# Performance work log

Hardware: AMD Instinct MI355X
Metric: run time of the kernel (lower is better)

Reference implementation:

```python
import jax, jax.numpy as jnp
import numpy as np

B, T, H, CH = 8192, 10, 512, 512  # batch, time_step, hidden_size, code_hidden_size (must be equal)


def setup_inputs() -> dict:
    key = jax.random.key(0)
    ks = jax.random.split(key, 18)
    s = 0.05
    inp = {
        "h": jax.random.normal(ks[0], (B, T, CH), dtype=jnp.float32),
        "y_seq": jax.random.normal(ks[1], (B, T), dtype=jnp.float32),
        "attn1_w": jax.random.normal(ks[2], (CH, 2 * H), dtype=jnp.float32) * s,
        "attn1_b": jax.random.normal(ks[3], (CH,), dtype=jnp.float32) * s,
        "attn2_w": jax.random.normal(ks[4], (CH, CH), dtype=jnp.float32) * s,
        "attn2_b": jax.random.normal(ks[5], (CH,), dtype=jnp.float32) * s,
        "attn3_w": jax.random.normal(ks[6], (1, CH), dtype=jnp.float32) * s,
        "attn3_b": jax.random.normal(ks[7], (1,), dtype=jnp.float32) * s,
        "W_ih": jax.random.normal(ks[8], (4 * H, 1), dtype=jnp.float32) * s,
        "W_hh": jax.random.normal(ks[9], (4 * H, H), dtype=jnp.float32) * s,
        "b_ih": jax.random.normal(ks[10], (4 * H,), dtype=jnp.float32) * s,
        "b_hh": jax.random.normal(ks[11], (4 * H,), dtype=jnp.float32) * s,
        "fc1_w": jax.random.normal(ks[12], (H, CH + H), dtype=jnp.float32) * s,
        "fc1_b": jax.random.normal(ks[13], (H,), dtype=jnp.float32) * s,
        "fc2_w": jax.random.normal(ks[14], (1, H), dtype=jnp.float32) * s,
        "fc2_b": jax.random.normal(ks[15], (1,), dtype=jnp.float32) * s,
    }
    return inp


def reference(h, y_seq, attn1_w, attn1_b, attn2_w, attn2_b, attn3_w, attn3_b,
              W_ih, W_hh, b_ih, b_hh, fc1_w, fc1_b, fc2_w, fc2_b):
    # h: [B, T, CH] -> scan over time; y_seq: [B, T]
    h_t = jnp.transpose(h, (1, 0, 2))      # [T, B, CH]
    y_t = jnp.transpose(y_seq, (1, 0))     # [T, B]
    b = h.shape[0]
    hid = W_hh.shape[1]
    d0 = jnp.zeros((b, hid), dtype=h.dtype)
    s0 = jnp.zeros((b, hid), dtype=h.dtype)

    def step(carry, xs):
        d, s = carry
        ht, yt = xs  # ht: [B, CH], yt: [B]
        # attention scores (note: original softmax is over a singleton dim -> weights == 1)
        x = jnp.concatenate([d, ht], axis=1)                       # [B, 2H]
        a = jnp.tanh((x @ attn1_w.T + attn1_b) @ attn2_w.T + attn2_b)
        w = a @ attn3_w.T + attn3_b                                # [B, 1]
        w = jax.nn.softmax(w, axis=1)                              # softmax over size-1 dim == 1
        h1 = w * ht                                                # [B, H] (CH == H)
        # single LSTM step with h0 = h1, c0 = s, input = yt (scalar feature)
        gates = yt[:, None] @ W_ih.T + b_ih + h1 @ W_hh.T + b_hh   # [B, 4H]
        i, f, g, o = jnp.split(gates, 4, axis=1)
        c = jax.nn.sigmoid(f) * s + jax.nn.sigmoid(i) * jnp.tanh(g)
        d_new = jax.nn.sigmoid(o) * jnp.tanh(c)
        return (d_new, c), None

    (d, s), _ = jax.lax.scan(step, (d0, s0), (h_t, y_t))
    z = jnp.concatenate([d, h_t[-1]], axis=1)                      # [B, CH+H]
    y_res = (z @ fc1_w.T + fc1_b) @ fc2_w.T + fc2_b                # [B, 1]
    return y_res
```

## Files before the change

kernel.cpp:

```cpp
#include <hip/hip_runtime.h>
#include <stdint.h>

typedef __attribute__((ext_vector_type(8))) short short8;
typedef __attribute__((ext_vector_type(4))) float f32x4;
typedef unsigned short ushort_t;

#define T_STEPS 10
#define BT  128
#define JPB 128
#define WPACK_BYTES (2048*1024)
#define VBUF_OFF  WPACK_BYTES
#define HBF_OFF   (WPACK_BYTES + 8192)
#define H_ELEMS   (8192ull*T_STEPS*512)
#define HBF_BYTES (H_ELEMS*2)

typedef const __attribute__((address_space(1))) void gas_void;
typedef __attribute__((address_space(3))) void las_void;

__device__ __forceinline__ void gld_lds16(const void* g, void* l){
  __builtin_amdgcn_global_load_lds((gas_void*)g, (las_void*)l, 16, 0, 0);
}

__device__ __forceinline__ unsigned int pk2(float x, float y){
  unsigned int bx = __float_as_uint(x), by = __float_as_uint(y);
  bx = (bx + 0x7FFFu + ((bx>>16)&1u)) >> 16;
  by = (by + 0x7FFFu + ((by>>16)&1u)) >> 16;
  return bx | (by<<16);
}
__device__ __forceinline__ float sigf(float x){ return 1.f/(1.f + __expf(-x)); }
__device__ __forceinline__ float tanh_(float x){
  x = fminf(fmaxf(x, -15.f), 15.f);
  float e = __expf(2.f*x);
  return (e - 1.f)/(e + 1.f);
}

__global__ __launch_bounds__(256) void k_pack(const float* __restrict__ Whh,
                                              ushort_t* __restrict__ wp){
  int id  = blockIdx.x*256 + threadIdx.x;
  int row = id >> 6;
  int ko  = (id & 63) * 8;
  const float* p = Whh + row*512 + ko;
  float4 a = *(const float4*)p, b = *(const float4*)(p+4);
  uint4 v;
  v.x = pk2(a.x,a.y); v.y = pk2(a.z,a.w);
  v.z = pk2(b.x,b.y); v.w = pk2(b.z,b.w);
  int g = row >> 9, j = row & 511;
  int jb = j >> 7, jt = (j >> 4) & 7, jl = j & 15;
  int kc = ko >> 5, khi = (ko >> 3) & 3, lane = khi*16 + jl;
  int chunk = ((jb*8 + jt)*4 + g)*16 + kc;
  *(uint4*)(wp + chunk*512 + lane*8) = v;
}

__global__ __launch_bounds__(256) void k_v(const float* __restrict__ fc1w,
                                           const float* __restrict__ fc1b,
                                           const float* __restrict__ fc2w,
                                           const float* __restrict__ fc2b,
                                           float* __restrict__ vout,
                                           float* __restrict__ bias0){
  __shared__ float red[4][64];
  int tid = threadIdx.x;
  if (blockIdx.x < 16){
    int j  = blockIdx.x*64 + (tid & 63);
    int hc = tid >> 6;
    float s = 0.f;
    for (int hh = hc*128; hh < hc*128 + 128; ++hh)
      s += fc2w[hh] * fc1w[hh*1024 + j];
    red[hc][tid & 63] = s;
    __syncthreads();
    if (tid < 64)
      vout[blockIdx.x*64 + tid] = red[0][tid]+red[1][tid]+red[2][tid]+red[3][tid];
  } else {
    if (tid < 64){
      float s = 0.f;
      for (int i = 0; i < 8; ++i){ int hh = i*64 + tid; s += fc2w[hh]*fc1b[hh]; }
      for (int m = 32; m; m >>= 1) s += __shfl_xor(s, m);
      if (tid == 0) *bias0 = s + fc2b[0];
    }
  }
}

__global__ __launch_bounds__(512) void k_init(const float* __restrict__ h,
                                              const float* __restrict__ v,
                                              const float* __restrict__ bias0,
                                              float* __restrict__ out){
  int w = threadIdx.x >> 6, lane = threadIdx.x & 63;
  float b0v = *bias0;
  const float* v2 = v + 512;
  for (int r = 0; r < 8; ++r){
    int b = blockIdx.x*64 + w*8 + r;
    const float* hp = h + ((size_t)b*T_STEPS + 9)*512 + lane*8;
    float4 x0 = *(const float4*)hp, x1 = *(const float4*)(hp+4);
    const float* vp = v2 + lane*8;
    float4 w0 = *(const float4*)vp, w1 = *(const float4*)(vp+4);
    float s = x0.x*w0.x + x0.y*w0.y + x0.z*w0.z + x0.w*w0.w
            + x1.x*w1.x + x1.y*w1.y + x1.z*w1.z + x1.w*w1.w;
    for (int m = 32; m; m >>= 1) s += __shfl_xor(s, m);
    if (lane == 0) out[b] = s + b0v;
  }
}

__global__ __launch_bounds__(256) void k_prep(const float* __restrict__ h,
                                              ushort_t* __restrict__ hbf){
  size_t id = (size_t)blockIdx.x*256 + threadIdx.x;
  if (id*16 >= H_ELEMS) return;
  const float* p = h + id*16;
  float4 a = *(const float4*)p,     b = *(const float4*)(p+4);
  float4 c = *(const float4*)(p+8), d = *(const float4*)(p+12);
  uint4 lo, hi;
  lo.x = pk2(a.x,a.y); lo.y = pk2(a.z,a.w); lo.z = pk2(b.x,b.y); lo.w = pk2(b.z,b.w);
  hi.x = pk2(c.x,c.y); hi.y = pk2(c.z,c.w); hi.z = pk2(d.x,d.y); hi.w = pk2(d.z,d.w);
  uint4* q = (uint4*)(hbf + id*16);
  q[0] = lo; q[1] = hi;
}

__device__ __forceinline__ void stage_prep(
    ushort_t* ab, ushort_t* wb, const ushort_t* __restrict__ hbf,
    const ushort_t* __restrict__ wpack, int b0, int jb, int s, int w, int lane)
{
  int t  = (s < 160) ? (s >> 4) : 9;
  int kc = s & 15;
  {
    int row = w*16 + (lane >> 2), qa = lane & 3;
    const ushort_t* src = hbf + ((size_t)(b0+row)*T_STEPS + t)*512 + kc*32 + qa*8;
    gld_lds16(src, ab + w*512);
  }
  if (s < 160){
#pragma unroll
    for (int i = 0; i < 3; ++i){
      int cw = w*3 + i, g = cw >> 3, jt = cw & 7;
      const ushort_t* src = wpack + ((size_t)((jb*8+jt)*4+g)*16 + kc)*512 + lane*8;
      gld_lds16(src, wb + (g*8+jt)*512);
    }
  } else {
    int jt = w;
    const ushort_t* src = wpack + ((size_t)((jb*8+jt)*4+3)*16 + kc)*512 + lane*8;
    gld_lds16(src, wb + jt*512);
  }
}

__device__ __forceinline__ void stage_sync(
    ushort_t* ab, ushort_t* wb, const float* __restrict__ h,
    const ushort_t* __restrict__ wpack, int b0, int jb, int s,
    int tid, int w, int lane)
{
  int t  = (s < 160) ? (s >> 4) : 9;
  int kc = s & 15;
  {
    int row = tid >> 2, qa = tid & 3;
    const float* p = h + ((size_t)(b0+row)*T_STEPS + t)*512 + kc*32 + qa*8;
    float4 x0 = *(const float4*)p, x1 = *(const float4*)(p+4);
    uint4 pk;
    pk.x = pk2(x0.x,x0.y); pk.y = pk2(x0.z,x0.w);
    pk.z = pk2(x1.x,x1.y); pk.w = pk2(x1.z,x1.w);
    *(uint4*)(ab + row*32 + qa*8) = pk;
  }
  if (s < 160){
#pragma unroll
    for (int i = 0; i < 3; ++i){
      int cw = w*3 + i, g = cw >> 3, jt = cw & 7;
      const ushort_t* src = wpack + ((size_t)((jb*8+jt)*4+g)*16 + kc)*512 + lane*8;
      gld_lds16(src, wb + (g*8+jt)*512);
    }
  } else {
    int jt = w;
    const ushort_t* src = wpack + ((size_t)((jb*8+jt)*4+3)*16 + kc)*512 + lane*8;
    gld_lds16(src, wb + jt*512);
  }
}

template<bool PREP>
__global__ __launch_bounds__(512) __attribute__((amdgpu_waves_per_eu(2)))
void k_main(const float* __restrict__ h, const ushort_t* __restrict__ hbf,
            const float* __restrict__ y,
            const float* __restrict__ Wih, const float* __restrict__ bih,
            const float* __restrict__ bhh,
            const ushort_t* __restrict__ wpack, const float* __restrict__ v1,
            float* __restrict__ out)
{
  __shared__ __align__(16) ushort_t Ab[2][BT*32];
  __shared__ __align__(16) ushort_t Wb[2][24*512];
  __shared__ float ys[BT*T_STEPS];

  int tid = threadIdx.x;
  int w = tid >> 6, lane = tid & 63, lhi = lane >> 4, llo = lane & 15;
  int mh = w & 1, wj = w >> 1;
  int bid = blockIdx.x;
  int xcd = bid & 7, q = bid >> 3;
  int tile = xcd*8 + (q >> 2), jb = q & 3;
  int b0 = tile * BT;

  float bias2[4][2], wihv[4][2];
#pragma unroll
  for (int g = 0; g < 4; ++g)
#pragma unroll
    for (int n = 0; n < 2; ++n){
      int col = g*512 + jb*128 + (wj*2+n)*16 + llo;
      bias2[g][n] = bih[col] + bhh[col];
      wihv[g][n]  = Wih[col];
    }

  for (int i = tid; i < BT*T_STEPS; i += 512)
    ys[i] = y[(size_t)b0*T_STEPS + i];

  if constexpr (PREP) stage_prep(Ab[0], Wb[0], hbf, wpack, b0, jb, 0, w, lane);
  else                stage_sync(Ab[0], Wb[0], h,   wpack, b0, jb, 0, tid, w, lane);
  __syncthreads();

  float cst[4][2][4];
  f32x4 acc[4][3][2];
#pragma unroll
  for (int m = 0; m < 4; ++m)
#pragma unroll
    for (int n = 0; n < 2; ++n){
#pragma unroll
      for (int r = 0; r < 4; ++r) cst[m][n][r] = 0.f;
#pragma unroll
      for (int g = 0; g < 3; ++g) acc[m][g][n] = (f32x4){0.f,0.f,0.f,0.f};
    }

#pragma unroll 1
  for (int s = 0; s < 160; ++s){
    int ns = s + 1;
    if constexpr (PREP) stage_prep(Ab[ns&1], Wb[ns&1], hbf, wpack, b0, jb, ns, w, lane);
    else                stage_sync(Ab[ns&1], Wb[ns&1], h,   wpack, b0, jb, ns, tid, w, lane);

    const ushort_t* ab = Ab[s&1];
    const ushort_t* wb = Wb[s&1];
    short8 af[4];
#pragma unroll
    for (int m = 0; m < 4; ++m){
      int row = mh*64 + m*16 + llo;
      af[m] = *(const short8*)(ab + row*32 + lhi*8);
    }
    short8 wf[3][2];
#pragma unroll
    for (int g = 0; g < 3; ++g)
#pragma unroll
      for (int n = 0; n < 2; ++n)
        wf[g][n] = *(const short8*)(wb + ((g*8 + wj*2 + n) << 9) + lane*8);
#pragma unroll
    for (int g = 0; g < 3; ++g)
#pragma unroll
      for (int n = 0; n < 2; ++n)
#pragma unroll
        for (int m = 0; m < 4; ++m)
          acc[m][g][n] = __builtin_amdgcn_mfma_f32_16x16x32_bf16(
              af[m], wf[g][n], acc[m][g][n], 0, 0, 0);

    if ((s & 15) == 15){
      int t = s >> 4;
#pragma unroll
      for (int m = 0; m < 4; ++m)
#pragma unroll
        for (int r = 0; r < 4; ++r){
          float yr = ys[(mh*64 + m*16 + lhi*4 + r)*T_STEPS + t];
#pragma unroll
          for (int n = 0; n < 2; ++n){
            float pi = acc[m][0][n][r] + fmaf(yr, wihv[0][n], bias2[0][n]);
            float pf = acc[m][1][n][r] + fmaf(yr, wihv[1][n], bias2[1][n]);
            float pg = acc[m][2][n][r] + fmaf(yr, wihv[2][n], bias2[2][n]);
            cst[m][n][r] = sigf(pf)*cst[m][n][r] + sigf(pi)*tanh_(pg);
          }
        }
#pragma unroll
      for (int m = 0; m < 4; ++m)
#pragma unroll
        for (int g = 0; g < 3; ++g)
#pragma unroll
          for (int n = 0; n < 2; ++n) acc[m][g][n] = (f32x4){0.f,0.f,0.f,0.f};
    }
    __syncthreads();
  }

  f32x4 acco[4][2];
#pragma unroll
  for (int m = 0; m < 4; ++m)
#pragma unroll
    for (int n = 0; n < 2; ++n) acco[m][n] = (f32x4){0.f,0.f,0.f,0.f};

#pragma unroll 1
  for (int s = 160; s < 176; ++s){
    if (s < 175){
      int ns = s + 1;
      if constexpr (PREP) stage_prep(Ab[ns&1], Wb[ns&1], hbf, wpack, b0, jb, ns, w, lane);
      else                stage_sync(Ab[ns&1], Wb[ns&1], h,   wpack, b0, jb, ns, tid, w, lane);
    }
    const ushort_t* ab = Ab[s&1];
    const ushort_t* wb = Wb[s&1];
    short8 af[4];
#pragma unroll
    for (int m = 0; m < 4; ++m){
      int row = mh*64 + m*16 + llo;
      af[m] = *(const short8*)(ab + row*32 + lhi*8);
    }
    short8 wo[2];
#pragma unroll
    for (int n = 0; n < 2; ++n)
      wo[n] = *(const short8*)(wb + ((wj*2 + n) << 9) + lane*8);
#pragma unroll
    for (int n = 0; n < 2; ++n)
#pragma unroll
      for (int m = 0; m < 4; ++m)
        acco[m][n] = __builtin_amdgcn_mfma_f32_16x16x32_bf16(
            af[m], wo[n], acco[m][n], 0, 0, 0);
    __syncthreads();
  }

  float v1v[2];
#pragma unroll
  for (int n = 0; n < 2; ++n) v1v[n] = v1[jb*128 + (wj*2+n)*16 + llo];

#pragma unroll
  for (int m = 0; m < 4; ++m)
#pragma unroll
    for (int r = 0; r < 4; ++r){
      float yr = ys[(mh*64 + m*16 + lhi*4 + r)*T_STEPS + 9];
      float val = 0.f;
#pragma unroll
      for (int n = 0; n < 2; ++n){
        float po = acco[m][n][r] + fmaf(yr, wihv[3][n], bias2[3][n]);
        val += sigf(po)*tanh_(cst[m][n][r])*v1v[n];
      }
      val += __shfl_xor(val, 1);
      val += __shfl_xor(val, 2);
      val += __shfl_xor(val, 4);
      val += __shfl_xor(val, 8);
      if (llo == 0)
        atomicAdd(&out[b0 + mh*64 + m*16 + lhi*4 + r], val);
    }
}

extern "C" void kernel_launch(void* const* d_in, const int* in_sizes, int n_in,
                              void* d_out, int out_size, void* d_ws, size_t ws_size,
                              hipStream_t stream){
  (void)in_sizes; (void)n_in; (void)out_size;
  const float* h    = (const float*)d_in[0];
  const float* y    = (const float*)d_in[1];
  const float* Wih  = (const float*)d_in[8];
  const float* Whh  = (const float*)d_in[9];
  const float* bih  = (const float*)d_in[10];
  const float* bhh  = (const float*)d_in[11];
  const float* fc1w = (const float*)d_in[12];
  const float* fc1b = (const float*)d_in[13];
  const float* fc2w = (const float*)d_in[14];
  const float* fc2b = (const float*)d_in[15];
  float* out = (float*)d_out;

  ushort_t* wpack = (ushort_t*)d_ws;
  float* vbuf  = (float*)((char*)d_ws + VBUF_OFF);
  float* bias0 = vbuf + 1024;
  ushort_t* hbf = (ushort_t*)((char*)d_ws + HBF_OFF);
  bool prep = ws_size >= (size_t)HBF_OFF + HBF_BYTES;

  k_pack<<<512, 256, 0, stream>>>(Whh, wpack);
  k_v<<<17, 256, 0, stream>>>(fc1w, fc1b, fc2w, fc2b, vbuf, bias0);
  if (prep){
    int prep_blocks = (int)(H_ELEMS / 16 / 256);
    k_prep<<<prep_blocks, 256, 0, stream>>>(h, hbf);
  }
  k_init<<<128, 512, 0, stream>>>(h, vbuf, bias0, out);
  if (prep)
    k_main<true ><<<256, 512, 0, stream>>>(h, hbf, y, Wih, bih, bhh, wpack, vbuf, out);
  else
    k_main<false><<<256, 512, 0, stream>>>(h, hbf, y, Wih, bih, bhh, wpack, vbuf, out);
}
```

Baseline: 287.7 us.

## Use 4-deep LDS ring with partial vmcnt waits in main GEMM loop

Replaces the double-buffered A/W staging with a 4-slot LDS ring, issuing global-to-LDS loads three stages ahead and waiting with explicit s_waitcnt vmcnt counts instead of a full __syncthreads drain each step. The recurrent and output-gate loops are merged into a single 176-step loop, and address bases are precomputed once. This aims to hide global memory latency behind MFMA work. In exchange it uses more LDS per block, and the hand-tuned wait counts must exactly match the number of outstanding loads.

```diff
diff --git a/kernel.cpp b/kernel.cpp
--- a/kernel.cpp
+++ b/kernel.cpp
@@ -7,7 +7,6 @@
 
 #define T_STEPS 10
 #define BT  128
-#define JPB 128
 #define WPACK_BYTES (2048*1024)
 #define VBUF_OFF  WPACK_BYTES
 #define HBF_OFF   (WPACK_BYTES + 8192)
@@ -20,6 +19,8 @@
 __device__ __forceinline__ void gld_lds16(const void* g, void* l){
   __builtin_amdgcn_global_load_lds((gas_void*)g, (las_void*)l, 16, 0, 0);
 }
+
+#define VMW(N) asm volatile("s_waitcnt vmcnt(" #N ")" ::: "memory")
 
 __device__ __forceinline__ unsigned int pk2(float x, float y){
   unsigned int bx = __float_as_uint(x), by = __float_as_uint(y);
@@ -109,76 +110,18 @@
   uint4 lo, hi;
   lo.x = pk2(a.x,a.y); lo.y = pk2(a.z,a.w); lo.z = pk2(b.x,b.y); lo.w = pk2(b.z,b.w);
   hi.x = pk2(c.x,c.y); hi.y = pk2(c.z,c.w); hi.z = pk2(d.x,d.y); hi.w = pk2(d.z,d.w);
-  uint4* q = (uint4*)(hbf + id*16);
-  q[0] = lo; q[1] = hi;
-}
-
-__device__ __forceinline__ void stage_prep(
-    ushort_t* ab, ushort_t* wb, const ushort_t* __restrict__ hbf,
-    const ushort_t* __restrict__ wpack, int b0, int jb, int s, int w, int lane)
+  uint4* qq = (uint4*)(hbf + id*16);
+  qq[0] = lo; qq[1] = hi;
+}
+
+__global__ __launch_bounds__(512) void k_main_p(
+    const ushort_t* __restrict__ hbf, const float* __restrict__ y,
+    const float* __restrict__ Wih, const float* __restrict__ bih,
+    const float* __restrict__ bhh,
+    const ushort_t* __restrict__ wpack, const float* __restrict__ v1,
+    float* __restrict__ out)
 {
-  int t  = (s < 160) ? (s >> 4) : 9;
-  int kc = s & 15;
-  {
-    int row = w*16 + (lane >> 2), qa = lane & 3;
-    const ushort_t* src = hbf + ((size_t)(b0+row)*T_STEPS + t)*512 + kc*32 + qa*8;
-    gld_lds16(src, ab + w*512);
-  }
-  if (s < 160){
-#pragma unroll
-    for (int i = 0; i < 3; ++i){
-      int cw = w*3 + i, g = cw >> 3, jt = cw & 7;
-      const ushort_t* src = wpack + ((size_t)((jb*8+jt)*4+g)*16 + kc)*512 + lane*8;
-      gld_lds16(src, wb + (g*8+jt)*512);
-    }
-  } else {
-    int jt = w;
-    const ushort_t* src = wpack + ((size_t)((jb*8+jt)*4+3)*16 + kc)*512 + lane*8;
-    gld_lds16(src, wb + jt*512);
-  }
-}
-
-__device__ __forceinline__ void stage_sync(
-    ushort_t* ab, ushort_t* wb, const float* __restrict__ h,
-    const ushort_t* __restrict__ wpack, int b0, int jb, int s,
-    int tid, int w, int lane)
-{
-  int t  = (s < 160) ? (s >> 4) : 9;
-  int kc = s & 15;
-  {
-    int row = tid >> 2, qa = tid & 3;
-    const float* p = h + ((size_t)(b0+row)*T_STEPS + t)*512 + kc*32 + qa*8;
-    float4 x0 = *(const float4*)p, x1 = *(const float4*)(p+4);
-    uint4 pk;
-    pk.x = pk2(x0.x,x0.y); pk.y = pk2(x0.z,x0.w);
-    pk.z = pk2(x1.x,x1.y); pk.w = pk2(x1.z,x1.w);
-    *(uint4*)(ab + row*32 + qa*8) = pk;
-  }
-  if (s < 160){
-#pragma unroll
-    for (int i = 0; i < 3; ++i){
-      int cw = w*3 + i, g = cw >> 3, jt = cw & 7;
-      const ushort_t* src = wpack + ((size_t)((jb*8+jt)*4+g)*16 + kc)*512 + lane*8;
-      gld_lds16(src, wb + (g*8+jt)*512);
-    }
-  } else {
-    int jt = w;
-    const ushort_t* src = wpack + ((size_t)((jb*8+jt)*4+3)*16 + kc)*512 + lane*8;
-    gld_lds16(src, wb + jt*512);
-  }
-}
-
-template<bool PREP>
-__global__ __launch_bounds__(512) __attribute__((amdgpu_waves_per_eu(2)))
-void k_main(const float* __restrict__ h, const ushort_t* __restrict__ hbf,
-            const float* __restrict__ y,
-            const float* __restrict__ Wih, const float* __restrict__ bih,
-            const float* __restrict__ bhh,
-            const ushort_t* __restrict__ wpack, const float* __restrict__ v1,
-            float* __restrict__ out)
-{
-  __shared__ __align__(16) ushort_t Ab[2][BT*32];
-  __shared__ __align__(16) ushort_t Wb[2][24*512];
+  __shared__ __align__(16) ushort_t ring[4][16384];
   __shared__ float ys[BT*T_STEPS];
 
   int tid = threadIdx.x;
@@ -189,6 +132,17 @@
   int tile = xcd*8 + (q >> 2), jb = q & 3;
   int b0 = tile * BT;
 
+  int cb[3];
+#pragma unroll
+  for (int i = 0; i < 3; ++i){
+    int cw = w*3 + i, g = cw >> 3, jt = cw & 7;
+    cb[i] = ((jb*8 + jt)*4 + g)*16;
+  }
+  int cbo = ((jb*8 + w)*4 + 3)*16;
+
+  int arow = w*16 + (lane >> 2), qa = lane & 3;
+  const ushort_t* asrc = hbf + ((size_t)(b0 + arow)*T_STEPS)*512 + qa*8;
+
   float bias2[4][2], wihv[4][2];
 #pragma unroll
   for (int g = 0; g < 4; ++g)
@@ -198,16 +152,31 @@
       bias2[g][n] = bih[col] + bhh[col];
       wihv[g][n]  = Wih[col];
     }
+  float v1v[2];
+#pragma unroll
+  for (int n = 0; n < 2; ++n) v1v[n] = v1[jb*128 + (wj*2+n)*16 + llo];
 
   for (int i = tid; i < BT*T_STEPS; i += 512)
     ys[i] = y[(size_t)b0*T_STEPS + i];
 
-  if constexpr (PREP) stage_prep(Ab[0], Wb[0], hbf, wpack, b0, jb, 0, w, lane);
-  else                stage_sync(Ab[0], Wb[0], h,   wpack, b0, jb, 0, tid, w, lane);
-  __syncthreads();
+#pragma unroll
+  for (int k = 0; k < 3; ++k){
+    ushort_t* base = ring[k];
+    gld_lds16(asrc, base + w*512);
+#pragma unroll
+    for (int i = 0; i < 3; ++i)
+      gld_lds16(wpack + (size_t)(cb[i] + k)*512 + lane*8,
+                base + 4096 + (w*3+i)*512);
+    asrc += 32;
+  }
+  asm volatile("s_waitcnt vmcnt(0) lgkmcnt(0)" ::: "memory");
+  __builtin_amdgcn_sched_barrier(0);
+  __builtin_amdgcn_s_barrier();
+  __builtin_amdgcn_sched_barrier(0);
 
   float cst[4][2][4];
   f32x4 acc[4][3][2];
+  f32x4 acco[4][2];
 #pragma unroll
   for (int m = 0; m < 4; ++m)
 #pragma unroll
@@ -216,99 +185,254 @@
       for (int r = 0; r < 4; ++r) cst[m][n][r] = 0.f;
 #pragma unroll
       for (int g = 0; g < 3; ++g) acc[m][g][n] = (f32x4){0.f,0.f,0.f,0.f};
+      acco[m][n] = (f32x4){0.f,0.f,0.f,0.f};
     }
 
 #pragma unroll 1
-  for (int s = 0; s < 160; ++s){
-    int ns = s + 1;
-    if constexpr (PREP) stage_prep(Ab[ns&1], Wb[ns&1], hbf, wpack, b0, jb, ns, w, lane);
-    else                stage_sync(Ab[ns&1], Wb[ns&1], h,   wpack, b0, jb, ns, tid, w, lane);
-
-    const ushort_t* ab = Ab[s&1];
-    const ushort_t* wb = Wb[s&1];
+  for (int s = 0; s < 176; ++s){
+    int ns = s + 3;
+    if (ns < 176){
+      if (ns == 160) asrc -= 512;
+      ushort_t* base = ring[ns & 3];
+      gld_lds16(asrc, base + w*512);
+      int kc = ns & 15;
+      if (ns < 160){
+#pragma unroll
+        for (int i = 0; i < 3; ++i)
+          gld_lds16(wpack + (size_t)(cb[i] + kc)*512 + lane*8,
+                    base + 4096 + (w*3+i)*512);
+      } else {
+        gld_lds16(wpack + (size_t)(cbo + kc)*512 + lane*8,
+                  base + 4096 + w*512);
+      }
+      asrc += 32;
+    }
+
+    const ushort_t* ab = ring[s & 3];
+    const ushort_t* wb = ab + 4096;
     short8 af[4];
 #pragma unroll
-    for (int m = 0; m < 4; ++m){
-      int row = mh*64 + m*16 + llo;
-      af[m] = *(const short8*)(ab + row*32 + lhi*8);
-    }
-    short8 wf[3][2];
-#pragma unroll
-    for (int g = 0; g < 3; ++g)
+    for (int m = 0; m < 4; ++m)
+      af[m] = *(const short8*)(ab + (mh*64 + m*16 + llo)*32 + lhi*8);
+
+    if (s < 160){
+      short8 wf[3][2];
+#pragma unroll
+      for (int g = 0; g < 3; ++g)
+#pragma unroll
+        for (int n = 0; n < 2; ++n)
+          wf[g][n] = *(const short8*)(wb + ((g*8 + wj*2 + n) << 9) + lane*8);
+#pragma unroll
+      for (int g = 0; g < 3; ++g)
+#pragma unroll
+        for (int n = 0; n < 2; ++n)
+#pragma unroll
+          for (int m = 0; m < 4; ++m)
+            acc[m][g][n] = __builtin_amdgcn_mfma_f32_16x16x32_bf16(
+                af[m], wf[g][n], acc[m][g][n], 0, 0, 0);
+      if ((s & 15) == 15){
+        int t = s >> 4;
+#pragma unroll
+        for (int m = 0; m < 4; ++m)
+#pragma unroll
+          for (int r = 0; r < 4; ++r){
+            float yr = ys[(mh*64 + m*16 + lhi*4 + r)*T_STEPS + t];
+#pragma unroll
+            for (int n = 0; n < 2; ++n){
+              float pi = acc[m][0][n][r] + fmaf(yr, wihv[0][n], bias2[0][n]);
+              float pf = acc[m][1][n][r] + fmaf(yr, wihv[1][n], bias2[1][n]);
+              float pg = acc[m][2][n][r] + fmaf(yr, wihv[2][n], bias2[2][n]);
+              cst[m][n][r] = sigf(pf)*cst[m][n][r] + sigf(pi)*tanh_(pg);
+            }
+          }
+#pragma unroll
+        for (int m = 0; m < 4; ++m)
+#pragma unroll
+          for (int g = 0; g < 3; ++g)
+#pragma unroll
+            for (int n = 0; n < 2; ++n) acc[m][g][n] = (f32x4){0.f,0.f,0.f,0.f};
+      }
+    } else {
+      short8 wo[2];
 #pragma unroll
       for (int n = 0; n < 2; ++n)
-        wf[g][n] = *(const short8*)(wb + ((g*8 + wj*2 + n) << 9) + lane*8);
-#pragma unroll
-    for (int g = 0; g < 3; ++g)
+        wo[n] = *(const short8*)(wb + ((wj*2 + n) << 9) + lane*8);
 #pragma unroll
       for (int n = 0; n < 2; ++n)
 #pragma unroll
         for (int m = 0; m < 4; ++m)
-          acc[m][g][n] = __builtin_amdgcn_mfma_f32_16x16x32_bf16(
-              af[m], wf[g][n], acc[m][g][n], 0, 0, 0);
-
-    if ((s & 15) == 15){
-      int t = s >> 4;
-#pragma unroll
-      for (int m = 0; m < 4; ++m)
-#pragma unroll
-        for (int r = 0; r < 4; ++r){
-          float yr = ys[(mh*64 + m*16 + lhi*4 + r)*T_STEPS + t];
-#pragma unroll
-          for (int n = 0; n < 2; ++n){
-            float pi = acc[m][0][n][r] + fmaf(yr, wihv[0][n], bias2[0][n]);
-            float pf = acc[m][1][n][r] + fmaf(yr, wihv[1][n], bias2[1][n]);
-            float pg = acc[m][2][n][r] + fmaf(yr, wihv[2][n], bias2[2][n]);
-            cst[m][n][r] = sigf(pf)*cst[m][n][r] + sigf(pi)*tanh_(pg);
+          acco[m][n] = __builtin_amdgcn_mfma_f32_16x16x32_bf16(
+              af[m], wo[n], acco[m][n], 0, 0, 0);
+    }
+
+    if (s <= 156)      { VMW(8); }
+    else if (s == 157) { VMW(6); }
+    else if (s <= 172) { VMW(4); }
+    else if (s == 173) { VMW(2); }
+    else               { VMW(0); }
+    __builtin_amdgcn_sched_barrier(0);
+    __builtin_amdgcn_s_barrier();
+    __builtin_amdgcn_sched_barrier(0);
+  }
+
+#pragma unroll
+  for (int m = 0; m < 4; ++m)
+#pragma unroll
+    for (int r = 0; r < 4; ++r){
+      float yr = ys[(mh*64 + m*16 + lhi*4 + r)*T_STEPS + 9];
+      float val = 0.f;
+#pragma unroll
+      for (int n = 0; n < 2; ++n){
+        float po = acco[m][n][r] + fmaf(yr, wihv[3][n], bias2[3][n]);
+        val += sigf(po)*tanh_(cst[m][n][r])*v1v[n];
+      }
+      val += __shfl_xor(val, 1);
+      val += __shfl_xor(val, 2);
+      val += __shfl_xor(val, 4);
+      val += __shfl_xor(val, 8);
+      if (llo == 0)
+        atomicAdd(&out[b0 + mh*64 + m*16 + lhi*4 + r], val);
+    }
+}
+
+__global__ __launch_bounds__(512) void k_main_f(
+    const float* __restrict__ h, const float* __restrict__ y,
+    const float* __restrict__ Wih, const float* __restrict__ bih,
+    const float* __restrict__ bhh,
+    const ushort_t* __restrict__ wpack, const float* __restrict__ v1,
+    float* __restrict__ out)
+{
+  __shared__ __align__(16) ushort_t ring[2][16384];
+  __shared__ float ys[BT*T_STEPS];
+
+  int tid = threadIdx.x;
+  int w = tid >> 6, lane = tid & 63, lhi = lane >> 4, llo = lane & 15;
+  int mh = w & 1, wj = w >> 1;
+  int bid = blockIdx.x;
+  int xcd = bid & 7, q = bid >> 3;
+  int tile = xcd*8 + (q >> 2), jb = q & 3;
+  int b0 = tile * BT;
+
+  float bias2[4][2], wihv[4][2];
+#pragma unroll
+  for (int g = 0; g < 4; ++g)
+#pragma unroll
+    for (int n = 0; n < 2; ++n){
+      int col = g*512 + jb*128 + (wj*2+n)*16 + llo;
+      bias2[g][n] = bih[col] + bhh[col];
+      wihv[g][n]  = Wih[col];
+    }
+  float v1v[2];
+#pragma unroll
+  for (int n = 0; n < 2; ++n) v1v[n] = v1[jb*128 + (wj*2+n)*16 + llo];
+
+  for (int i = tid; i < BT*T_STEPS; i += 512)
+    ys[i] = y[(size_t)b0*T_STEPS + i];
+
+  auto stage = [&](ushort_t* base, int s){
+    int t  = (s < 160) ? (s >> 4) : 9;
+    int kc = s & 15;
+    {
+      int row = tid >> 2, qa2 = tid & 3;
+      const float* p = h + ((size_t)(b0+row)*T_STEPS + t)*512 + kc*32 + qa2*8;
+      float4 x0 = *(const float4*)p, x1 = *(const float4*)(p+4);
+      uint4 pk;
+      pk.x = pk2(x0.x,x0.y); pk.y = pk2(x0.z,x0.w);
+      pk.z = pk2(x1.x,x1.y); pk.w = pk2(x1.z,x1.w);
+      *(uint4*)(base + row*32 + qa2*8) = pk;
+    }
+    if (s < 160){
+#pragma unroll
+      for (int i = 0; i < 3; ++i){
+        int cw = w*3 + i, g = cw >> 3, jt = cw & 7;
+        gld_lds16(wpack + ((size_t)((jb*8+jt)*4+g)*16 + kc)*512 + lane*8,
+                  base + 4096 + cw*512);
+      }
+    } else {
+      gld_lds16(wpack + ((size_t)((jb*8+w)*4+3)*16 + kc)*512 + lane*8,
+                base + 4096 + w*512);
+    }
+  };
+
+  stage(ring[0], 0);
+  __syncthreads();
+
+  float cst[4][2][4];
+  f32x4 acc[4][3][2];
+  f32x4 acco[4][2];
+#pragma unroll
+  for (int m = 0; m < 4; ++m)
+#pragma unroll
+    for (int n = 0; n < 2; ++n){
+#pragma unroll
+      for (int r = 0; r < 4; ++r) cst[m][n][r] = 0.f;
+#pragma unroll
+      for (int g = 0; g < 3; ++g) acc[m][g][n] = (f32x4){0.f,0.f,0.f,0.f};
+      acco[m][n] = (f32x4){0.f,0.f,0.f,0.f};
+    }
+
+#pragma unroll 1
+  for (int s = 0; s < 176; ++s){
+    if (s + 1 < 176) stage(ring[(s+1)&1], s+1);
+
+    const ushort_t* ab = ring[s & 1];
+    const ushort_t* wb = ab + 4096;
+    short8 af[4];
+#pragma unroll
+    for (int m = 0; m < 4; ++m)
+      af[m] = *(const short8*)(ab + (mh*64 + m*16 + llo)*32 + lhi*8);
+
+    if (s < 160){
+      short8 wf[3][2];
+#pragma unroll
+      for (int g = 0; g < 3; ++g)
+#pragma unroll
+        for (int n = 0; n < 2; ++n)
+          wf[g][n] = *(const short8*)(wb + ((g*8 + wj*2 + n) << 9) + lane*8);
+#pragma unroll
+      for (int g = 0; g < 3; ++g)
+#pragma unroll
+        for (int n = 0; n < 2; ++n)
+#pragma unroll
+          for (int m = 0; m < 4; ++m)
+            acc[m][g][n] = __builtin_amdgcn_mfma_f32_16x16x32_bf16(
+                af[m], wf[g][n], acc[m][g][n], 0, 0, 0);
+      if ((s & 15) == 15){
+        int t = s >> 4;
+#pragma unroll
+        for (int m = 0; m < 4; ++m)
+#pragma unroll
+          for (int r = 0; r < 4; ++r){
+            float yr = ys[(mh*64 + m*16 + lhi*4 + r)*T_STEPS + t];
+#pragma unroll
+            for (int n = 0; n < 2; ++n){
+              float pi = acc[m][0][n][r] + fmaf(yr, wihv[0][n], bias2[0][n]);
+              float pf = acc[m][1][n][r] + fmaf(yr, wihv[1][n], bias2[1][n]);
+              float pg = acc[m][2][n][r] + fmaf(yr, wihv[2][n], bias2[2][n]);
+              cst[m][n][r] = sigf(pf)*cst[m][n][r] + sigf(pi)*tanh_(pg);
+            }
           }
-        }
-#pragma unroll
-      for (int m = 0; m < 4; ++m)
-#pragma unroll
-        for (int g = 0; g < 3; ++g)
-#pragma unroll
-          for (int n = 0; n < 2; ++n) acc[m][g][n] = (f32x4){0.f,0.f,0.f,0.f};
+#pragma unroll
+        for (int m = 0; m < 4; ++m)
+#pragma unroll
+          for (int g = 0; g < 3; ++g)
+#pragma unroll
+            for (int n = 0; n < 2; ++n) acc[m][g][n] = (f32x4){0.f,0.f,0.f,0.f};
+      }
+    } else {
+      short8 wo[2];
+#pragma unroll
+      for (int n = 0; n < 2; ++n)
+        wo[n] = *(const short8*)(wb + ((wj*2 + n) << 9) + lane*8);
+#pragma unroll
+      for (int n = 0; n < 2; ++n)
+#pragma unroll
+        for (int m = 0; m < 4; ++m)
+          acco[m][n] = __builtin_amdgcn_mfma_f32_16x16x32_bf16(
+              af[m], wo[n], acco[m][n], 0, 0, 0);
     }
     __syncthreads();
   }
-
-  f32x4 acco[4][2];
-#pragma unroll
-  for (int m = 0; m < 4; ++m)
-#pragma unroll
-    for (int n = 0; n < 2; ++n) acco[m][n] = (f32x4){0.f,0.f,0.f,0.f};
-
-#pragma unroll 1
-  for (int s = 160; s < 176; ++s){
-    if (s < 175){
-      int ns = s + 1;
-      if constexpr (PREP) stage_prep(Ab[ns&1], Wb[ns&1], hbf, wpack, b0, jb, ns, w, lane);
-      else                stage_sync(Ab[ns&1], Wb[ns&1], h,   wpack, b0, jb, ns, tid, w, lane);
-    }
-    const ushort_t* ab = Ab[s&1];
-    const ushort_t* wb = Wb[s&1];
-    short8 af[4];
-#pragma unroll
-    for (int m = 0; m < 4; ++m){
-      int row = mh*64 + m*16 + llo;
-      af[m] = *(const short8*)(ab + row*32 + lhi*8);
-    }
-    short8 wo[2];
-#pragma unroll
-    for (int n = 0; n < 2; ++n)
-      wo[n] = *(const short8*)(wb + ((wj*2 + n) << 9) + lane*8);
-#pragma unroll
-    for (int n = 0; n < 2; ++n)
-#pragma unroll
-      for (int m = 0; m < 4; ++m)
-        acco[m][n] = __builtin_amdgcn_mfma_f32_16x16x32_bf16(
-            af[m], wo[n], acco[m][n], 0, 0, 0);
-    __syncthreads();
-  }
-
-  float v1v[2];
-#pragma unroll
-  for (int n = 0; n < 2; ++n) v1v[n] = v1[jb*128 + (wj*2+n)*16 + llo];
 
 #pragma unroll
   for (int m = 0; m < 4; ++m)
@@ -360,7 +484,7 @@
   }
   k_init<<<128, 512, 0, stream>>>(h, vbuf, bias0, out);
   if (prep)
-    k_main<true ><<<256, 512, 0, stream>>>(h, hbf, y, Wih, bih, bhh, wpack, vbuf, out);
+    k_main_p<<<256, 512, 0, stream>>>(hbf, y, Wih, bih, bhh, wpack, vbuf, out);
   else
-    k_main<false><<<256, 512, 0, stream>>>(h, hbf, y, Wih, bih, bhh, wpack, vbuf, out);
-}
+    k_main_f<<<256, 512, 0, stream>>>(h, y, Wih, bih, bhh, wpack, vbuf, out);
+}
```

Measured after the change: 295.0 us. 2.5% more time.

## Stage full-timestep activations in swizzled LDS and stream weights from global

Applied to the files above, without the earlier changes.

The main kernel now stages a whole timestep's 128x512 bf16 activation tile in LDS, split into two halves with an XOR swizzle. Each half of the next timestep is loaded while the other half is being computed, so block-wide barriers drop from one per 32-wide K chunk to two per timestep. Weight fragments are no longer staged through LDS; each wave reads them directly from global memory (L2) inside the unrolled MFMA loop. The o-gate pass reuses the already resident last-timestep tile instead of streaming it again. The cost is a 128KB LDS footprint that limits occupancy, plus global-load latency on the weight fragments with no explicit prefetch.

```diff
diff --git a/kernel.cpp b/kernel.cpp
--- a/kernel.cpp
+++ b/kernel.cpp
@@ -6,8 +6,7 @@
 typedef unsigned short ushort_t;
 
 #define T_STEPS 10
-#define BT  128
-#define JPB 128
+#define BT 128
 #define WPACK_BYTES (2048*1024)
 #define VBUF_OFF  WPACK_BYTES
 #define HBF_OFF   (WPACK_BYTES + 8192)
@@ -109,76 +108,106 @@
   uint4 lo, hi;
   lo.x = pk2(a.x,a.y); lo.y = pk2(a.z,a.w); lo.z = pk2(b.x,b.y); lo.w = pk2(b.z,b.w);
   hi.x = pk2(c.x,c.y); hi.y = pk2(c.z,c.w); hi.z = pk2(d.x,d.y); hi.w = pk2(d.z,d.w);
-  uint4* q = (uint4*)(hbf + id*16);
-  q[0] = lo; q[1] = hi;
-}
-
-__device__ __forceinline__ void stage_prep(
-    ushort_t* ab, ushort_t* wb, const ushort_t* __restrict__ hbf,
-    const ushort_t* __restrict__ wpack, int b0, int jb, int s, int w, int lane)
-{
-  int t  = (s < 160) ? (s >> 4) : 9;
-  int kc = s & 15;
-  {
-    int row = w*16 + (lane >> 2), qa = lane & 3;
-    const ushort_t* src = hbf + ((size_t)(b0+row)*T_STEPS + t)*512 + kc*32 + qa*8;
-    gld_lds16(src, ab + w*512);
-  }
-  if (s < 160){
-#pragma unroll
-    for (int i = 0; i < 3; ++i){
-      int cw = w*3 + i, g = cw >> 3, jt = cw & 7;
-      const ushort_t* src = wpack + ((size_t)((jb*8+jt)*4+g)*16 + kc)*512 + lane*8;
-      gld_lds16(src, wb + (g*8+jt)*512);
-    }
-  } else {
-    int jt = w;
-    const ushort_t* src = wpack + ((size_t)((jb*8+jt)*4+3)*16 + kc)*512 + lane*8;
-    gld_lds16(src, wb + jt*512);
-  }
-}
-
-__device__ __forceinline__ void stage_sync(
-    ushort_t* ab, ushort_t* wb, const float* __restrict__ h,
-    const ushort_t* __restrict__ wpack, int b0, int jb, int s,
-    int tid, int w, int lane)
-{
-  int t  = (s < 160) ? (s >> 4) : 9;
-  int kc = s & 15;
-  {
-    int row = tid >> 2, qa = tid & 3;
-    const float* p = h + ((size_t)(b0+row)*T_STEPS + t)*512 + kc*32 + qa*8;
+  uint4* qq = (uint4*)(hbf + id*16);
+  qq[0] = lo; qq[1] = hi;
+}
+
+__device__ __forceinline__ void stage_half_prep(
+    ushort_t* As, const ushort_t* __restrict__ hbf,
+    int b0, int t, int kh, int w, int lane)
+{
+  int rl = lane >> 5, lk = lane & 31;
+#pragma unroll
+  for (int r = 0; r < 8; ++r){
+    int row = r*16 + w*2 + rl;
+    const ushort_t* src = hbf + ((size_t)(b0+row)*T_STEPS + t)*512 + kh*256
+                        + ((lk ^ (row & 7)) * 8);
+    gld_lds16(src, As + (size_t)kh*32768 + (r*16 + w*2)*256);
+  }
+}
+
+__device__ __forceinline__ void stage_half_sync(
+    ushort_t* As, const float* __restrict__ h,
+    int b0, int t, int kh, int tid)
+{
+  int w = tid >> 6, lane = tid & 63, rl = lane >> 5, lk = lane & 31;
+#pragma unroll
+  for (int r = 0; r < 8; ++r){
+    int row = r*16 + w*2 + rl;
+    const float* p = h + ((size_t)(b0+row)*T_STEPS + t)*512 + kh*256
+                   + ((lk ^ (row & 7)) * 8);
     float4 x0 = *(const float4*)p, x1 = *(const float4*)(p+4);
     uint4 pk;
     pk.x = pk2(x0.x,x0.y); pk.y = pk2(x0.z,x0.w);
     pk.z = pk2(x1.x,x1.y); pk.w = pk2(x1.z,x1.w);
-    *(uint4*)(ab + row*32 + qa*8) = pk;
-  }
-  if (s < 160){
-#pragma unroll
-    for (int i = 0; i < 3; ++i){
-      int cw = w*3 + i, g = cw >> 3, jt = cw & 7;
-      const ushort_t* src = wpack + ((size_t)((jb*8+jt)*4+g)*16 + kc)*512 + lane*8;
-      gld_lds16(src, wb + (g*8+jt)*512);
-    }
-  } else {
-    int jt = w;
-    const ushort_t* src = wpack + ((size_t)((jb*8+jt)*4+3)*16 + kc)*512 + lane*8;
-    gld_lds16(src, wb + jt*512);
+    *(uint4*)(As + (size_t)kh*32768 + row*256 + lk*8) = pk;
+  }
+}
+
+__device__ __forceinline__ void gate_8(
+    const ushort_t* __restrict__ As8, const ushort_t* __restrict__ wpack,
+    int cb, int kb, int mh, int llo, int lhi, int lane,
+    f32x4 (&acc)[4][3][2])
+{
+#pragma unroll
+  for (int kl = 0; kl < 8; ++kl){
+    short8 wf[3][2];
+#pragma unroll
+    for (int g = 0; g < 3; ++g)
+#pragma unroll
+      for (int n = 0; n < 2; ++n)
+        wf[g][n] = *(const short8*)&wpack[(size_t)(cb + (n*4+g)*16 + kb + kl)*512 + lane*8];
+    short8 af[4];
+#pragma unroll
+    for (int m = 0; m < 4; ++m)
+      af[m] = *(const short8*)&As8[(mh*64 + m*16 + llo)*256
+                                   + ((kl*32 + lhi*8) ^ ((llo & 7) << 3))];
+#pragma unroll
+    for (int g = 0; g < 3; ++g)
+#pragma unroll
+      for (int n = 0; n < 2; ++n)
+#pragma unroll
+        for (int m = 0; m < 4; ++m)
+          acc[m][g][n] = __builtin_amdgcn_mfma_f32_16x16x32_bf16(
+              af[m], wf[g][n], acc[m][g][n], 0, 0, 0);
+  }
+}
+
+__device__ __forceinline__ void ogate_8(
+    const ushort_t* __restrict__ As8, const ushort_t* __restrict__ wpack,
+    int cb, int kb, int mh, int llo, int lhi, int lane,
+    f32x4 (&acco)[4][2])
+{
+#pragma unroll
+  for (int kl = 0; kl < 8; ++kl){
+    short8 wo[2];
+#pragma unroll
+    for (int n = 0; n < 2; ++n)
+      wo[n] = *(const short8*)&wpack[(size_t)(cb + (n*4+3)*16 + kb + kl)*512 + lane*8];
+    short8 af[4];
+#pragma unroll
+    for (int m = 0; m < 4; ++m)
+      af[m] = *(const short8*)&As8[(mh*64 + m*16 + llo)*256
+                                   + ((kl*32 + lhi*8) ^ ((llo & 7) << 3))];
+#pragma unroll
+    for (int n = 0; n < 2; ++n)
+#pragma unroll
+      for (int m = 0; m < 4; ++m)
+        acco[m][n] = __builtin_amdgcn_mfma_f32_16x16x32_bf16(
+            af[m], wo[n], acco[m][n], 0, 0, 0);
   }
 }
 
 template<bool PREP>
-__global__ __launch_bounds__(512) __attribute__((amdgpu_waves_per_eu(2)))
-void k_main(const float* __restrict__ h, const ushort_t* __restrict__ hbf,
-            const float* __restrict__ y,
-            const float* __restrict__ Wih, const float* __restrict__ bih,
-            const float* __restrict__ bhh,
-            const ushort_t* __restrict__ wpack, const float* __restrict__ v1,
-            float* __restrict__ out)
-{
-  __shared__ __align__(16) ushort_t Ab[2][BT*32];
-  __shared__ __align__(16) ushort_t Wb[2][24*512];
+__global__ __launch_bounds__(512) void k_main(
+    const float* __restrict__ h, const ushort_t* __restrict__ hbf,
+    const float* __restrict__ y,
+    const float* __restrict__ Wih, const float* __restrict__ bih,
+    const float* __restrict__ bhh,
+    const ushort_t* __restrict__ wpack, const float* __restrict__ v1,
+    float* __restrict__ out)
+{
+  __shared__ __align__(16) ushort_t As[2*128*256];
   __shared__ float ys[BT*T_STEPS];
 
   int tid = threadIdx.x;
@@ -188,6 +217,7 @@
   int xcd = bid & 7, q = bid >> 3;
   int tile = xcd*8 + (q >> 2), jb = q & 3;
   int b0 = tile * BT;
+  int cb = (jb*8 + wj*2)*4*16;
 
   float bias2[4][2], wihv[4][2];
 #pragma unroll
@@ -198,78 +228,69 @@
       bias2[g][n] = bih[col] + bhh[col];
       wihv[g][n]  = Wih[col];
     }
+  float v1v[2];
+#pragma unroll
+  for (int n = 0; n < 2; ++n) v1v[n] = v1[jb*128 + (wj*2+n)*16 + llo];
 
   for (int i = tid; i < BT*T_STEPS; i += 512)
     ys[i] = y[(size_t)b0*T_STEPS + i];
 
-  if constexpr (PREP) stage_prep(Ab[0], Wb[0], hbf, wpack, b0, jb, 0, w, lane);
-  else                stage_sync(Ab[0], Wb[0], h,   wpack, b0, jb, 0, tid, w, lane);
+  if constexpr (PREP){
+    stage_half_prep(As, hbf, b0, 0, 0, w, lane);
+    stage_half_prep(As, hbf, b0, 0, 1, w, lane);
+  } else {
+    stage_half_sync(As, h, b0, 0, 0, tid);
+    stage_half_sync(As, h, b0, 0, 1, tid);
+  }
   __syncthreads();
 
+  f32x4 acc[4][3][2];
   float cst[4][2][4];
-  f32x4 acc[4][3][2];
 #pragma unroll
   for (int m = 0; m < 4; ++m)
 #pragma unroll
     for (int n = 0; n < 2; ++n){
 #pragma unroll
+      for (int g = 0; g < 3; ++g) acc[m][g][n] = (f32x4){0.f,0.f,0.f,0.f};
+#pragma unroll
       for (int r = 0; r < 4; ++r) cst[m][n][r] = 0.f;
-#pragma unroll
-      for (int g = 0; g < 3; ++g) acc[m][g][n] = (f32x4){0.f,0.f,0.f,0.f};
     }
 
 #pragma unroll 1
-  for (int s = 0; s < 160; ++s){
-    int ns = s + 1;
-    if constexpr (PREP) stage_prep(Ab[ns&1], Wb[ns&1], hbf, wpack, b0, jb, ns, w, lane);
-    else                stage_sync(Ab[ns&1], Wb[ns&1], h,   wpack, b0, jb, ns, tid, w, lane);
-
-    const ushort_t* ab = Ab[s&1];
-    const ushort_t* wb = Wb[s&1];
-    short8 af[4];
-#pragma unroll
-    for (int m = 0; m < 4; ++m){
-      int row = mh*64 + m*16 + llo;
-      af[m] = *(const short8*)(ab + row*32 + lhi*8);
-    }
-    short8 wf[3][2];
-#pragma unroll
-    for (int g = 0; g < 3; ++g)
-#pragma unroll
-      for (int n = 0; n < 2; ++n)
-        wf[g][n] = *(const short8*)(wb + ((g*8 + wj*2 + n) << 9) + lane*8);
-#pragma unroll
-    for (int g = 0; g < 3; ++g)
-#pragma unroll
-      for (int n = 0; n < 2; ++n)
-#pragma unroll
-        for (int m = 0; m < 4; ++m)
-          acc[m][g][n] = __builtin_amdgcn_mfma_f32_16x16x32_bf16(
-              af[m], wf[g][n], acc[m][g][n], 0, 0, 0);
-
-    if ((s & 15) == 15){
-      int t = s >> 4;
-#pragma unroll
-      for (int m = 0; m < 4; ++m)
-#pragma unroll
-        for (int r = 0; r < 4; ++r){
-          float yr = ys[(mh*64 + m*16 + lhi*4 + r)*T_STEPS + t];
-#pragma unroll
-          for (int n = 0; n < 2; ++n){
-            float pi = acc[m][0][n][r] + fmaf(yr, wihv[0][n], bias2[0][n]);
-            float pf = acc[m][1][n][r] + fmaf(yr, wihv[1][n], bias2[1][n]);
-            float pg = acc[m][2][n][r] + fmaf(yr, wihv[2][n], bias2[2][n]);
-            cst[m][n][r] = sigf(pf)*cst[m][n][r] + sigf(pi)*tanh_(pg);
-          }
+  for (int t = 0; t < T_STEPS; ++t){
+    gate_8(As, wpack, cb, 0, mh, llo, lhi, lane, acc);
+    __syncthreads();
+    if (t < T_STEPS-1){
+      if constexpr (PREP) stage_half_prep(As, hbf, b0, t+1, 0, w, lane);
+      else                stage_half_sync(As, h,   b0, t+1, 0, tid);
+    }
+    gate_8(As + 32768, wpack, cb, 8, mh, llo, lhi, lane, acc);
+
+#pragma unroll
+    for (int m = 0; m < 4; ++m)
+#pragma unroll
+      for (int r = 0; r < 4; ++r){
+        float yr = ys[(mh*64 + m*16 + lhi*4 + r)*T_STEPS + t];
+#pragma unroll
+        for (int n = 0; n < 2; ++n){
+          float pi = acc[m][0][n][r] + fmaf(yr, wihv[0][n], bias2[0][n]);
+          float pf = acc[m][1][n][r] + fmaf(yr, wihv[1][n], bias2[1][n]);
+          float pg = acc[m][2][n][r] + fmaf(yr, wihv[2][n], bias2[2][n]);
+          cst[m][n][r] = sigf(pf)*cst[m][n][r] + sigf(pi)*tanh_(pg);
         }
-#pragma unroll
-      for (int m = 0; m < 4; ++m)
-#pragma unroll
-        for (int g = 0; g < 3; ++g)
-#pragma unroll
-          for (int n = 0; n < 2; ++n) acc[m][g][n] = (f32x4){0.f,0.f,0.f,0.f};
-    }
+      }
+#pragma unroll
+    for (int m = 0; m < 4; ++m)
+#pragma unroll
+      for (int g = 0; g < 3; ++g)
+#pragma unroll
+        for (int n = 0; n < 2; ++n) acc[m][g][n] = (f32x4){0.f,0.f,0.f,0.f};
+
     __syncthreads();
+    if (t < T_STEPS-1){
+      if constexpr (PREP) stage_half_prep(As, hbf, b0, t+1, 1, w, lane);
+      else                stage_half_sync(As, h,   b0, t+1, 1, tid);
+    }
   }
 
   f32x4 acco[4][2];
@@ -277,38 +298,8 @@
   for (int m = 0; m < 4; ++m)
 #pragma unroll
     for (int n = 0; n < 2; ++n) acco[m][n] = (f32x4){0.f,0.f,0.f,0.f};
-
-#pragma unroll 1
-  for (int s = 160; s < 176; ++s){
-    if (s < 175){
-      int ns = s + 1;
-      if constexpr (PREP) stage_prep(Ab[ns&1], Wb[ns&1], hbf, wpack, b0, jb, ns, w, lane);
-      else                stage_sync(Ab[ns&1], Wb[ns&1], h,   wpack, b0, jb, ns, tid, w, lane);
-    }
-    const ushort_t* ab = Ab[s&1];
-    const ushort_t* wb = Wb[s&1];
-    short8 af[4];
-#pragma unroll
-    for (int m = 0; m < 4; ++m){
-      int row = mh*64 + m*16 + llo;
-      af[m] = *(const short8*)(ab + row*32 + lhi*8);
-    }
-    short8 wo[2];
-#pragma unroll
-    for (int n = 0; n < 2; ++n)
-      wo[n] = *(const short8*)(wb + ((wj*2 + n) << 9) + lane*8);
-#pragma unroll
-    for (int n = 0; n < 2; ++n)
-#pragma unroll
-      for (int m = 0; m < 4; ++m)
-        acco[m][n] = __builtin_amdgcn_mfma_f32_16x16x32_bf16(
-            af[m], wo[n], acco[m][n], 0, 0, 0);
-    __syncthreads();
-  }
-
-  float v1v[2];
-#pragma unroll
-  for (int n = 0; n < 2; ++n) v1v[n] = v1[jb*128 + (wj*2+n)*16 + llo];
+  ogate_8(As,         wpack, cb, 0, mh, llo, lhi, lane, acco);
+  ogate_8(As + 32768, wpack, cb, 8, mh, llo, lhi, lane, acco);
 
 #pragma unroll
   for (int m = 0; m < 4; ++m)
```

After: 726.2 us. 2.52x slower.
